# Kernel tuning notes

Hardware: AMD Instinct MI355X
Metric: run time of the kernel (lower is better)

Reference implementation:

```python
import jax, jax.numpy as jnp
import numpy as np
from jax import lax

N = 8192
D = 128
CHUNK = 128  # rows of adj processed per scan step; bounds the [CHUNK, N, D] masked intermediate


def setup_inputs() -> dict:
    key = jax.random.key(0)
    k1, k2 = jax.random.split(key)
    x = jax.random.normal(k1, (N, D), dtype=jnp.float32)
    adj = jax.random.randint(k2, (N, N), 0, 2, dtype=jnp.int32)
    return {"x": x, "adj": adj}


def reference(x, adj):
    # For each node i: max over features of its neighbors (adj[i] nonzero),
    # or zeros if it has no neighbors. Equivalent to a masked row-max.
    n, d = x.shape
    neg = jnp.finfo(x.dtype).min
    adj_chunks = adj.reshape(n // CHUNK, CHUNK, n)

    def step(carry, a):  # a: [CHUNK, n]
        mask = a != 0
        # masked: [CHUNK, n, d] — neighbors keep x, non-neighbors get -inf-like
        masked = jnp.where(mask[:, :, None], x[None, :, :], neg)
        m = jnp.max(masked, axis=1)                      # [CHUNK, d]
        has_nbr = jnp.any(mask, axis=1)                  # [CHUNK]
        out = jnp.where(has_nbr[:, None], m, jnp.zeros((), x.dtype))
        return carry, out

    _, out = lax.scan(step, None, adj_chunks)
    return out.reshape(n, d)
```

## Files before the change

kernel.cpp:

```cpp
#include <hip/hip_runtime.h>
#include <cfloat>
#include <cstdint>

#define NN 8192
#define DD 128
#define W64PR 128
#define TOPK 32

__device__ __forceinline__ uint32_t f2s(float f) {
  uint32_t u = __float_as_uint(f);
  return (u & 0x80000000u) ? ~u : (u | 0x80000000u);
}
__device__ __forceinline__ float s2f(uint32_t s) {
  return (s & 0x80000000u) ? __uint_as_float(s & 0x7fffffffu)
                           : __uint_as_float(~s);
}


__global__ __launch_bounds__(256) void prep_kernel(
    const float* __restrict__ x, const int* __restrict__ adj,
    unsigned long long* __restrict__ bits, int* __restrict__ has_nbr,
    float2* __restrict__ tk) {
  const int b = blockIdx.x;
  const int t = threadIdx.x;
  const int lane = t & 63;
  const int wv = t >> 6;

  __shared__ unsigned long long red[4];
  __shared__ unsigned long long bcast;
  __shared__ int anyflag;

  if (b >= DD) {
    const int row = b - DD;
    const uint4* src = (const uint4*)(adj + (size_t)row * NN);
    unsigned long long* dst = bits + (size_t)row * W64PR;
    if (t == 0) anyflag = 0;
    __syncthreads();
    unsigned long long any = 0;
#pragma unroll
    for (int c = 0; c < 8; ++c) {
      uint4 v = src[c * 256 + t];
      unsigned long long b0 = __ballot(v.x != 0);
      unsigned long long b1 = __ballot(v.y != 0);
      unsigned long long b2 = __ballot(v.z != 0);
      unsigned long long b3 = __ballot(v.w != 0);
      any |= (b0 | b1 | b2 | b3);
      if (lane == 0) {
        ulonglong2* p = (ulonglong2*)(dst + (c * 16 + wv * 4));
        ulonglong2 q0; q0.x = b0; q0.y = b1;
        ulonglong2 q1; q1.x = b2; q1.y = b3;
        p[0] = q0;
        p[1] = q1;
      }
    }
    if (lane == 0 && any) anyflag = 1;
    __syncthreads();
    if (t == 0) has_nbr[row] = anyflag;
  } else {
    const int d = b;
    unsigned long long key[32];
#pragma unroll
    for (int e = 0; e < 32; ++e) {
      int j = t * 32 + e;
      key[e] = ((unsigned long long)f2s(x[(size_t)j * DD + d]) << 32) | (unsigned)j;
    }
    unsigned long long prev = ~0ull;
    for (int k = 0; k < TOPK; ++k) {
      unsigned long long best = 0ull;
#pragma unroll
      for (int e = 0; e < 32; ++e)
        if (key[e] < prev && key[e] > best) best = key[e];
      for (int off = 32; off; off >>= 1) {
        unsigned long long o = __shfl_down(best, off, 64);
        if (o > best) best = o;
      }
      if (lane == 0) red[wv] = best;
      __syncthreads();
      if (t == 0) {
        unsigned long long m = red[0];
        for (int i = 1; i < 4; ++i) if (red[i] > m) m = red[i];
        bcast = m;
        float2 kv;
        kv.x = s2f((uint32_t)(m >> 32));
        kv.y = __int_as_float((int)(uint32_t)(m & 0xffffffffu));
        tk[k * DD + d] = kv;
      }
      __syncthreads();
      prev = bcast;
    }
  }
}

__global__ __launch_bounds__(256) void probe_kernel(
    const float* __restrict__ x, const unsigned long long* __restrict__ bits,
    const int* __restrict__ has_nbr, const float2* __restrict__ tk,
    float* __restrict__ out) {
  const int t = threadIdx.x;
  const int row = blockIdx.x * 2 + (t >> 7);
  const int d = t & 127;
  const uint32_t* rb32 = (const uint32_t*)(bits + (size_t)row * W64PR);

  float res = 0.0f;
  bool done = false;
  for (int k = 0; k < TOPK; ++k) {
    float2 kv = tk[k * DD + d];
    int idx = __float_as_int(kv.y);
    int i64 = ((idx >> 10) << 4) | (((idx >> 8) & 3) << 2) | (idx & 3);
    int l = (idx >> 2) & 63;
    uint32_t w = rb32[i64 * 2 + (l >> 5)];
    bool hit = (w >> (l & 31)) & 1u;
    if (!done && hit) { res = kv.x; done = true; }
    if (__all((int)done)) break;
  }
  if (__any((int)(!done))) {
    if (!done && has_nbr[row]) {
      float m = -FLT_MAX;
      const unsigned long long* rb64 = bits + (size_t)row * W64PR;
      for (int i = 0; i < W64PR; ++i) {
        unsigned long long bm = rb64[i];
        int base = ((i >> 4) << 10) + (((i >> 2) & 3) << 8) + (i & 3);
        while (bm) {
          int l2 = __ffsll((unsigned long long)bm) - 1;
          bm &= bm - 1;
          int j = base + 4 * l2;
          m = fmaxf(m, x[(size_t)j * DD + d]);
        }
      }
      res = m;
    }
  }
  out[(size_t)row * DD + d] = res;
}

extern "C" void kernel_launch(void* const* d_in, const int* in_sizes, int n_in,
                              void* d_out, int out_size, void* d_ws, size_t ws_size,
                              hipStream_t stream) {
  const float* x = (const float*)d_in[0];
  const int* adj = (const int*)d_in[1];
  float* out = (float*)d_out;

  unsigned long long* bits = (unsigned long long*)d_ws;
  int* has_nbr = (int*)((char*)d_ws + (size_t)NN * W64PR * 8);
  float2* tk = (float2*)((char*)has_nbr + (size_t)NN * 4);

  prep_kernel<<<NN + DD, 256, 0, stream>>>(x, adj, bits, has_nbr, tk);
  probe_kernel<<<NN / 2, 256, 0, stream>>>(x, bits, has_nbr, tk, out);
}
```

Measured before the change: 374.8 us.

## Drop adjacency bit-packing pass and probe adj directly for top-k hits

Removes the full pass that converted the 256MB int32 adjacency matrix into bitmasks and per-row neighbor flags. The probe kernel now reads adj entries directly at the indices of each feature's top-32 values, so for random dense inputs only a few scattered reads per row are needed instead of streaming the whole matrix. The fallback path scans the full adj row serially per thread, which would be very slow if it triggers, and the top-k kernel now runs on only 128 blocks with nothing to overlap it.

```diff
diff --git a/kernel.cpp b/kernel.cpp
--- a/kernel.cpp
+++ b/kernel.cpp
@@ -4,7 +4,6 @@
 
 #define NN 8192
 #define DD 128
-#define W64PR 128
 #define TOPK 32
 
 __device__ __forceinline__ uint32_t f2s(float f) {
@@ -16,117 +15,74 @@
                            : __uint_as_float(~s);
 }
 
-
-__global__ __launch_bounds__(256) void prep_kernel(
-    const float* __restrict__ x, const int* __restrict__ adj,
-    unsigned long long* __restrict__ bits, int* __restrict__ has_nbr,
-    float2* __restrict__ tk) {
-  const int b = blockIdx.x;
+__global__ __launch_bounds__(256) void topk_kernel(
+    const float* __restrict__ x, float2* __restrict__ tk) {
+  const int d = blockIdx.x;
   const int t = threadIdx.x;
   const int lane = t & 63;
   const int wv = t >> 6;
 
   __shared__ unsigned long long red[4];
   __shared__ unsigned long long bcast;
-  __shared__ int anyflag;
 
-  if (b >= DD) {
-    const int row = b - DD;
-    const uint4* src = (const uint4*)(adj + (size_t)row * NN);
-    unsigned long long* dst = bits + (size_t)row * W64PR;
-    if (t == 0) anyflag = 0;
+  unsigned long long key[32];
+#pragma unroll
+  for (int e = 0; e < 32; ++e) {
+    int j = t * 32 + e;
+    key[e] = ((unsigned long long)f2s(x[(size_t)j * DD + d]) << 32) | (unsigned)j;
+  }
+  unsigned long long prev = ~0ull;
+  for (int k = 0; k < TOPK; ++k) {
+    unsigned long long best = 0ull;
+#pragma unroll
+    for (int e = 0; e < 32; ++e)
+      if (key[e] < prev && key[e] > best) best = key[e];
+    for (int off = 32; off; off >>= 1) {
+      unsigned long long o = __shfl_down(best, off, 64);
+      if (o > best) best = o;
+    }
+    if (lane == 0) red[wv] = best;
     __syncthreads();
-    unsigned long long any = 0;
-#pragma unroll
-    for (int c = 0; c < 8; ++c) {
-      uint4 v = src[c * 256 + t];
-      unsigned long long b0 = __ballot(v.x != 0);
-      unsigned long long b1 = __ballot(v.y != 0);
-      unsigned long long b2 = __ballot(v.z != 0);
-      unsigned long long b3 = __ballot(v.w != 0);
-      any |= (b0 | b1 | b2 | b3);
-      if (lane == 0) {
-        ulonglong2* p = (ulonglong2*)(dst + (c * 16 + wv * 4));
-        ulonglong2 q0; q0.x = b0; q0.y = b1;
-        ulonglong2 q1; q1.x = b2; q1.y = b3;
-        p[0] = q0;
-        p[1] = q1;
-      }
+    if (t == 0) {
+      unsigned long long m = red[0];
+      for (int i = 1; i < 4; ++i) if (red[i] > m) m = red[i];
+      bcast = m;
+      float2 kv;
+      kv.x = s2f((uint32_t)(m >> 32));
+      kv.y = __int_as_float((int)(uint32_t)(m & 0xffffffffu));
+      tk[k * DD + d] = kv;
     }
-    if (lane == 0 && any) anyflag = 1;
     __syncthreads();
-    if (t == 0) has_nbr[row] = anyflag;
-  } else {
-    const int d = b;
-    unsigned long long key[32];
-#pragma unroll
-    for (int e = 0; e < 32; ++e) {
-      int j = t * 32 + e;
-      key[e] = ((unsigned long long)f2s(x[(size_t)j * DD + d]) << 32) | (unsigned)j;
-    }
-    unsigned long long prev = ~0ull;
-    for (int k = 0; k < TOPK; ++k) {
-      unsigned long long best = 0ull;
-#pragma unroll
-      for (int e = 0; e < 32; ++e)
-        if (key[e] < prev && key[e] > best) best = key[e];
-      for (int off = 32; off; off >>= 1) {
-        unsigned long long o = __shfl_down(best, off, 64);
-        if (o > best) best = o;
-      }
-      if (lane == 0) red[wv] = best;
-      __syncthreads();
-      if (t == 0) {
-        unsigned long long m = red[0];
-        for (int i = 1; i < 4; ++i) if (red[i] > m) m = red[i];
-        bcast = m;
-        float2 kv;
-        kv.x = s2f((uint32_t)(m >> 32));
-        kv.y = __int_as_float((int)(uint32_t)(m & 0xffffffffu));
-        tk[k * DD + d] = kv;
-      }
-      __syncthreads();
-      prev = bcast;
-    }
+    prev = bcast;
   }
 }
 
 __global__ __launch_bounds__(256) void probe_kernel(
-    const float* __restrict__ x, const unsigned long long* __restrict__ bits,
-    const int* __restrict__ has_nbr, const float2* __restrict__ tk,
-    float* __restrict__ out) {
+    const float* __restrict__ x, const int* __restrict__ adj,
+    const float2* __restrict__ tk, float* __restrict__ out) {
   const int t = threadIdx.x;
   const int row = blockIdx.x * 2 + (t >> 7);
   const int d = t & 127;
-  const uint32_t* rb32 = (const uint32_t*)(bits + (size_t)row * W64PR);
+  const int* __restrict__ arow = adj + (size_t)row * NN;
 
   float res = 0.0f;
   bool done = false;
   for (int k = 0; k < TOPK; ++k) {
-    float2 kv = tk[k * DD + d];
-    int idx = __float_as_int(kv.y);
-    int i64 = ((idx >> 10) << 4) | (((idx >> 8) & 3) << 2) | (idx & 3);
-    int l = (idx >> 2) & 63;
-    uint32_t w = rb32[i64 * 2 + (l >> 5)];
-    bool hit = (w >> (l & 31)) & 1u;
-    if (!done && hit) { res = kv.x; done = true; }
+    if (!done) {
+      float2 kv = tk[k * DD + d];
+      int idx = __float_as_int(kv.y);
+      if (arow[idx] != 0) { res = kv.x; done = true; }
+    }
     if (__all((int)done)) break;
   }
   if (__any((int)(!done))) {
-    if (!done && has_nbr[row]) {
+    if (!done) {
       float m = -FLT_MAX;
-      const unsigned long long* rb64 = bits + (size_t)row * W64PR;
-      for (int i = 0; i < W64PR; ++i) {
-        unsigned long long bm = rb64[i];
-        int base = ((i >> 4) << 10) + (((i >> 2) & 3) << 8) + (i & 3);
-        while (bm) {
-          int l2 = __ffsll((unsigned long long)bm) - 1;
-          bm &= bm - 1;
-          int j = base + 4 * l2;
-          m = fmaxf(m, x[(size_t)j * DD + d]);
-        }
+      bool any = false;
+      for (int j = 0; j < NN; ++j) {
+        if (arow[j] != 0) { any = true; m = fmaxf(m, x[(size_t)j * DD + d]); }
       }
-      res = m;
+      res = any ? m : 0.0f;
     }
   }
   out[(size_t)row * DD + d] = res;
@@ -139,10 +95,8 @@
   const int* adj = (const int*)d_in[1];
   float* out = (float*)d_out;
 
-  unsigned long long* bits = (unsigned long long*)d_ws;
-  int* has_nbr = (int*)((char*)d_ws + (size_t)NN * W64PR * 8);
-  float2* tk = (float2*)((char*)has_nbr + (size_t)NN * 4);
+  float2* tk = (float2*)d_ws;
 
-  prep_kernel<<<NN + DD, 256, 0, stream>>>(x, adj, bits, has_nbr, tk);
-  probe_kernel<<<NN / 2, 256, 0, stream>>>(x, bits, has_nbr, tk, out);
+  topk_kernel<<<DD, 256, 0, stream>>>(x, tk);
+  probe_kernel<<<NN / 2, 256, 0, stream>>>(x, adj, tk, out);
 }
```

After: 391.1 us. 4.4% more time.
